# Kernel optimization log

Hardware: AMD Instinct MI355X
Metric: run time of the kernel (lower is better)

## Reference

```python
import jax, jax.numpy as jnp
import numpy as np

M = 0.25
S = 64.0  # gamma
OP = 1.0 + M      # optimum for positives
ON = -M           # optimum for negatives
DELTA_P = 1.0 - M
DELTA_N = M
EPS = 1e-12       # F.normalize eps

B, D, C = 256, 512, 100000


def setup_inputs() -> dict:
    key = jax.random.key(0)
    k1, k2, k3, k4 = jax.random.split(key, 4)
    x = jax.random.normal(k1, (B, D), dtype=jnp.float32)
    emb = jax.random.normal(k2, (B, D), dtype=jnp.float32)
    W = jax.random.normal(k3, (C, D), dtype=jnp.float32) * 0.02  # fc.weight [C, D]
    labels = jax.random.randint(k4, (B,), 0, C, dtype=jnp.int64)
    return {"x": x, "labels": labels, "emb": emb, "W": W}


def reference(x, labels, emb, W):
    # x is unused in the original forward (dead argument)
    # F.normalize(emb): L2-normalize rows with eps clamp
    norm = jnp.linalg.norm(emb, axis=1, keepdims=True)
    ff = emb / jnp.maximum(norm, EPS)
    # fc(ff): linear classifier (weights NOT normalized; the torch loop is a no-op)
    wf = ff @ W.T  # [B, C]
    wf_d = jax.lax.stop_gradient(wf)

    rows = jnp.arange(wf.shape[0])
    sp_logit = wf[rows, labels]        # torch.diagonal(wf.T[labels])
    sp_logit_d = wf_d[rows, labels]

    alpha_p = jnp.maximum(OP - sp_logit_d, 0.0)          # clamp_min(-s_p + Op, 0)
    sp = jnp.exp(-S * alpha_p * (sp_logit - DELTA_P))    # [B]

    # negatives: all classes except the label column (mask instead of cat-slicing)
    neg_mask = jnp.asarray(rows[:, None] >= 0, wf.dtype) * (1.0 - jax.nn.one_hot(labels, wf.shape[1], dtype=wf.dtype))
    alpha_n = jnp.maximum(wf_d + M, 0.0)                 # clamp_min(s_n - On, 0)
    sn = jnp.exp(S * alpha_n * (wf - DELTA_N)) * neg_mask  # label column zeroed out

    loss = jnp.log(1.0 + sn.sum() * sp.sum())
    return loss
```

## Files before the change

kernel.cpp:

```cpp
#include <hip/hip_runtime.h>
#include <hip/hip_bf16.h>

typedef __attribute__((ext_vector_type(8))) __bf16 bf16x8;
typedef __attribute__((ext_vector_type(4))) float f32x4;

#define B_M 256
#define K_D 512
#define N_C 100000
#define BN 64
#define BK 64
#define NBLK ((N_C + BN - 1) / BN)

__device__ __forceinline__ unsigned short f2bf(float x) {
  unsigned int u = __float_as_uint(x);
  u += 0x7fffu + ((u >> 16) & 1u);
  return (unsigned short)(u >> 16);
}

__global__ __launch_bounds__(256) void norm_kernel(const float* __restrict__ emb,
                                                   unsigned short* __restrict__ ff) {
  const int row = blockIdx.x;
  const int t = threadIdx.x;
  float a = emb[row * K_D + t];
  float b = emb[row * K_D + t + 256];
  float ss = a * a + b * b;
  #pragma unroll
  for (int o = 32; o > 0; o >>= 1) ss += __shfl_down(ss, o, 64);
  __shared__ float red[4];
  const int wid = t >> 6, lane = t & 63;
  if (lane == 0) red[wid] = ss;
  __syncthreads();
  float tot = red[0] + red[1] + red[2] + red[3];
  float rn = 1.0f / fmaxf(sqrtf(tot), 1e-12f);
  ff[row * K_D + t]       = f2bf(a * rn);
  ff[row * K_D + t + 256] = f2bf(b * rn);
}

__global__ __launch_bounds__(512) void gemm_loss_kernel(const unsigned short* __restrict__ ff,
                                                        const float* __restrict__ W,
                                                        const int* __restrict__ labels,
                                                        double* __restrict__ partials) {
  __shared__ __align__(16) unsigned short As[B_M * BK];
  __shared__ __align__(16) unsigned short Bs[BN * BK];
  __shared__ int lbl[B_M];
  __shared__ double red[16];

  const int tid = threadIdx.x;
  const int wid = tid >> 6;
  const int lane = tid & 63;
  const int n0 = blockIdx.x * BN;

  if (tid < B_M) lbl[tid] = labels[tid];

  f32x4 acc[2][4] = {};

  const int wrow = wid * 32;
  const int l15 = lane & 15;
  const int lhi = lane >> 4;

  const int bcol = tid >> 3;
  const int bk8  = tid & 7;
  const long long jrow = (long long)n0 + bcol;

  for (int kk = 0; kk < K_D / BK; ++kk) {
    if (kk) __syncthreads();
    #pragma unroll
    for (int it = 0; it < 4; ++it) {
      int idx = it * 512 + tid;
      int row = idx >> 3;
      int kc  = idx & 7;
      uint4 v = *reinterpret_cast<const uint4*>(ff + row * K_D + kk * BK + kc * 8);
      int off = (row * 128 + kc * 16) ^ ((row & 7) << 4);
      *reinterpret_cast<uint4*>(reinterpret_cast<char*>(As) + off) = v;
    }
    {
      float4 f0 = {0.f, 0.f, 0.f, 0.f}, f1 = {0.f, 0.f, 0.f, 0.f};
      if (jrow < N_C) {
        const float* gp = W + jrow * K_D + kk * BK + bk8 * 8;
        f0 = *reinterpret_cast<const float4*>(gp);
        f1 = *reinterpret_cast<const float4*>(gp + 4);
      }
      union { unsigned short us[8]; uint4 v; } pk;
      pk.us[0] = f2bf(f0.x); pk.us[1] = f2bf(f0.y); pk.us[2] = f2bf(f0.z); pk.us[3] = f2bf(f0.w);
      pk.us[4] = f2bf(f1.x); pk.us[5] = f2bf(f1.y); pk.us[6] = f2bf(f1.z); pk.us[7] = f2bf(f1.w);
      int off = (bcol * 128 + bk8 * 16) ^ ((bcol & 7) << 4);
      *reinterpret_cast<uint4*>(reinterpret_cast<char*>(Bs) + off) = pk.v;
    }
    __syncthreads();

    bf16x8 afr[2][2], bfr[4][2];
    #pragma unroll
    for (int fm = 0; fm < 2; ++fm)
      #pragma unroll
      for (int ks = 0; ks < 2; ++ks) {
        int row = wrow + fm * 16 + l15;
        int off = (row * 128 + ks * 64 + lhi * 16) ^ ((row & 7) << 4);
        afr[fm][ks] = *reinterpret_cast<const bf16x8*>(reinterpret_cast<const char*>(As) + off);
      }
    #pragma unroll
    for (int fn = 0; fn < 4; ++fn)
      #pragma unroll
      for (int ks = 0; ks < 2; ++ks) {
        int col = fn * 16 + l15;
        int off = (col * 128 + ks * 64 + lhi * 16) ^ ((col & 7) << 4);
        bfr[fn][ks] = *reinterpret_cast<const bf16x8*>(reinterpret_cast<const char*>(Bs) + off);
      }
    #pragma unroll
    for (int fm = 0; fm < 2; ++fm)
      #pragma unroll
      for (int fn = 0; fn < 4; ++fn)
        #pragma unroll
        for (int ks = 0; ks < 2; ++ks)
          acc[fm][fn] = __builtin_amdgcn_mfma_f32_16x16x32_bf16(afr[fm][ks], bfr[fn][ks], acc[fm][fn], 0, 0, 0);
  }

  float sn_local = 0.0f;
  double sp_local = 0.0;
  #pragma unroll
  for (int fm = 0; fm < 2; ++fm)
    #pragma unroll
    for (int fn = 0; fn < 4; ++fn)
      #pragma unroll
      for (int r = 0; r < 4; ++r) {
        int row = wrow + fm * 16 + lhi * 4 + r;
        int j = n0 + fn * 16 + l15;
        float v = acc[fm][fn][r];
        if (j < N_C) {
          if (j == lbl[row]) {
            double alpha = fmax(1.25 - (double)v, 0.0);
            sp_local += exp(-64.0 * alpha * ((double)v - 0.75));
          } else {
            float an = fmaxf(v + 0.25f, 0.0f);
            sn_local += __expf(64.0f * an * (v - 0.25f));
          }
        }
      }

  double sn_d = (double)sn_local;
  #pragma unroll
  for (int o = 32; o > 0; o >>= 1) {
    sn_d     += __shfl_down(sn_d, o, 64);
    sp_local += __shfl_down(sp_local, o, 64);
  }
  if (lane == 0) { red[wid] = sn_d; red[8 + wid] = sp_local; }
  __syncthreads();
  if (tid == 0) {
    double a = 0.0, b = 0.0;
    #pragma unroll
    for (int i = 0; i < 8; ++i) { a += red[i]; b += red[8 + i]; }
    partials[blockIdx.x] = a;
    partials[NBLK + blockIdx.x] = b;
  }
}

__global__ __launch_bounds__(512) void finalize_kernel(const double* __restrict__ partials,
                                                       float* __restrict__ out) {
  const int t = threadIdx.x;
  double sn = 0.0, sp = 0.0;
  for (int i = t; i < NBLK; i += 512) { sn += partials[i]; sp += partials[NBLK + i]; }
  #pragma unroll
  for (int o = 32; o > 0; o >>= 1) { sn += __shfl_down(sn, o, 64); sp += __shfl_down(sp, o, 64); }
  __shared__ double red[16];
  const int wid = t >> 6, lane = t & 63;
  if (lane == 0) { red[wid] = sn; red[8 + wid] = sp; }
  __syncthreads();
  if (t == 0) {
    double a = 0.0, b = 0.0;
    for (int i = 0; i < 8; ++i) { a += red[i]; b += red[8 + i]; }
    out[0] = (float)log1p(a * b);
  }
}

extern "C" void kernel_launch(void* const* d_in, const int* in_sizes, int n_in,
                              void* d_out, int out_size, void* d_ws, size_t ws_size,
                              hipStream_t stream) {
  const int*   labels = (const int*)d_in[1];
  const float* emb    = (const float*)d_in[2];
  const float* W      = (const float*)d_in[3];
  float* out = (float*)d_out;

  unsigned short* ff = (unsigned short*)d_ws;
  double* partials = (double*)((char*)d_ws + (size_t)B_M * K_D * 2);

  norm_kernel<<<B_M, 256, 0, stream>>>(emb, ff);
  gemm_loss_kernel<<<NBLK, 512, 0, stream>>>(ff, W, labels, partials);
  finalize_kernel<<<1, 512, 0, stream>>>(partials, out);
}
```

Before: 73.61 us.

## Double-buffer GEMM tiles, split batch rows across blocks, load A via global_load_lds

The fused GEMM+loss kernel now double-buffers both LDS tiles. The W fp32 loads for the next K step are issued before the current step's MFMAs and converted to bf16 afterwards, so global latency overlaps compute. The 256-row batch is split into two 128-row blocks per column tile, doubling the grid. The normalized-embedding tile is copied straight into LDS with global_load_lds, using a pre-swizzled source address. The cost is that each W tile is read and converted twice, by the two M-blocks, which relies on the cache to absorb the extra traffic. LDS use also grows.

```diff
diff --git a/kernel.cpp b/kernel.cpp
--- a/kernel.cpp
+++ b/kernel.cpp
@@ -7,14 +7,23 @@
 #define B_M 256
 #define K_D 512
 #define N_C 100000
+#define BM 128
 #define BN 64
 #define BK 64
-#define NBLK ((N_C + BN - 1) / BN)
+#define NSTEP (K_D / BK)
+#define NB_N ((N_C + BN - 1) / BN)
+#define NB (2 * NB_N)
 
 __device__ __forceinline__ unsigned short f2bf(float x) {
   unsigned int u = __float_as_uint(x);
   u += 0x7fffu + ((u >> 16) & 1u);
   return (unsigned short)(u >> 16);
+}
+
+__device__ __forceinline__ void glds16(const void* g, void* l) {
+  __builtin_amdgcn_global_load_lds(
+      (const __attribute__((address_space(1))) unsigned int*)g,
+      (__attribute__((address_space(3))) unsigned int*)l, 16, 0, 0);
 }
 
 __global__ __launch_bounds__(256) void norm_kernel(const float* __restrict__ emb,
@@ -40,93 +49,119 @@
                                                         const float* __restrict__ W,
                                                         const int* __restrict__ labels,
                                                         double* __restrict__ partials) {
-  __shared__ __align__(16) unsigned short As[B_M * BK];
-  __shared__ __align__(16) unsigned short Bs[BN * BK];
-  __shared__ int lbl[B_M];
+  __shared__ __align__(16) unsigned short As[2][BM * BK];
+  __shared__ __align__(16) unsigned short Bs[2][BN * BK];
+  __shared__ int lbl[BM];
   __shared__ double red[16];
 
   const int tid = threadIdx.x;
   const int wid = tid >> 6;
   const int lane = tid & 63;
-  const int n0 = blockIdx.x * BN;
-
-  if (tid < B_M) lbl[tid] = labels[tid];
-
-  f32x4 acc[2][4] = {};
-
-  const int wrow = wid * 32;
   const int l15 = lane & 15;
   const int lhi = lane >> 4;
 
+  const int bid = blockIdx.x;
+  const int nb = bid >> 1;
+  const int mb = bid & 1;
+  const int n0 = nb * BN;
+  const int m0 = mb * BM;
+
+  if (tid < BM) lbl[tid] = labels[m0 + tid];
+
+  const int mq = wid & 3;
+  const int nq = wid >> 2;
+
   const int bcol = tid >> 3;
   const int bk8  = tid & 7;
-  const long long jrow = (long long)n0 + bcol;
-
-  for (int kk = 0; kk < K_D / BK; ++kk) {
-    if (kk) __syncthreads();
+  const int jglob = n0 + bcol;
+  const bool valid = jglob < N_C;
+  const float* wp = W + (long long)(valid ? jglob : (N_C - 1)) * K_D + bk8 * 8;
+  const int woff = (bcol * 128 + bk8 * 16) ^ ((bcol & 7) << 4);
+
+  const int s0 = tid, s1 = 512 + tid;
+  const int arow0 = s0 >> 3, ak0 = (s0 & 7) ^ (arow0 & 7);
+  const int arow1 = s1 >> 3, ak1 = (s1 & 7) ^ (arow1 & 7);
+  const unsigned short* ap0 = ff + (m0 + arow0) * K_D + ak0 * 8;
+  const unsigned short* ap1 = ff + (m0 + arow1) * K_D + ak1 * 8;
+
+  f32x4 acc[2][2] = {};
+
+  {
+    float4 w0 = *reinterpret_cast<const float4*>(wp);
+    float4 w1 = *reinterpret_cast<const float4*>(wp + 4);
+    glds16(ap0, &As[0][0] + (size_t)s0 * 8);
+    glds16(ap1, &As[0][0] + (size_t)s1 * 8);
+    union { unsigned short us[8]; uint4 v; } pk;
+    pk.us[0] = f2bf(w0.x); pk.us[1] = f2bf(w0.y); pk.us[2] = f2bf(w0.z); pk.us[3] = f2bf(w0.w);
+    pk.us[4] = f2bf(w1.x); pk.us[5] = f2bf(w1.y); pk.us[6] = f2bf(w1.z); pk.us[7] = f2bf(w1.w);
+    *reinterpret_cast<uint4*>(reinterpret_cast<char*>(&Bs[0][0]) + woff) = pk.v;
+    asm volatile("s_waitcnt vmcnt(0)" ::: "memory");
+    asm volatile("s_waitcnt lgkmcnt(0)" ::: "memory");
+    __builtin_amdgcn_s_barrier();
+  }
+
+  for (int t = 0; t < NSTEP; ++t) {
+    const int cur = t & 1;
+    const int nxt = cur ^ 1;
+    const bool stage = (t + 1 < NSTEP);
+
+    float4 w0n, w1n;
+    if (stage) {
+      w0n = *reinterpret_cast<const float4*>(wp + (t + 1) * BK);
+      w1n = *reinterpret_cast<const float4*>(wp + (t + 1) * BK + 4);
+      glds16(ap0 + (t + 1) * BK, &As[nxt][0] + (size_t)s0 * 8);
+      glds16(ap1 + (t + 1) * BK, &As[nxt][0] + (size_t)s1 * 8);
+    }
+
+    const char* ab = reinterpret_cast<const char*>(&As[cur][0]);
+    const char* bb = reinterpret_cast<const char*>(&Bs[cur][0]);
     #pragma unroll
-    for (int it = 0; it < 4; ++it) {
-      int idx = it * 512 + tid;
-      int row = idx >> 3;
-      int kc  = idx & 7;
-      uint4 v = *reinterpret_cast<const uint4*>(ff + row * K_D + kk * BK + kc * 8);
-      int off = (row * 128 + kc * 16) ^ ((row & 7) << 4);
-      *reinterpret_cast<uint4*>(reinterpret_cast<char*>(As) + off) = v;
+    for (int ks = 0; ks < 2; ++ks) {
+      bf16x8 afr[2], bfr[2];
+      #pragma unroll
+      for (int fm = 0; fm < 2; ++fm) {
+        int row = mq * 32 + fm * 16 + l15;
+        int off = row * 128 + (((ks * 4 + lhi) ^ (row & 7)) << 4);
+        afr[fm] = *reinterpret_cast<const bf16x8*>(ab + off);
+      }
+      #pragma unroll
+      for (int fn = 0; fn < 2; ++fn) {
+        int col = nq * 32 + fn * 16 + l15;
+        int off = col * 128 + (((ks * 4 + lhi) ^ (col & 7)) << 4);
+        bfr[fn] = *reinterpret_cast<const bf16x8*>(bb + off);
+      }
+      #pragma unroll
+      for (int fm = 0; fm < 2; ++fm)
+        #pragma unroll
+        for (int fn = 0; fn < 2; ++fn)
+          acc[fm][fn] = __builtin_amdgcn_mfma_f32_16x16x32_bf16(afr[fm], bfr[fn], acc[fm][fn], 0, 0, 0);
     }
-    {
-      float4 f0 = {0.f, 0.f, 0.f, 0.f}, f1 = {0.f, 0.f, 0.f, 0.f};
-      if (jrow < N_C) {
-        const float* gp = W + jrow * K_D + kk * BK + bk8 * 8;
-        f0 = *reinterpret_cast<const float4*>(gp);
-        f1 = *reinterpret_cast<const float4*>(gp + 4);
-      }
+
+    if (stage) {
       union { unsigned short us[8]; uint4 v; } pk;
-      pk.us[0] = f2bf(f0.x); pk.us[1] = f2bf(f0.y); pk.us[2] = f2bf(f0.z); pk.us[3] = f2bf(f0.w);
-      pk.us[4] = f2bf(f1.x); pk.us[5] = f2bf(f1.y); pk.us[6] = f2bf(f1.z); pk.us[7] = f2bf(f1.w);
-      int off = (bcol * 128 + bk8 * 16) ^ ((bcol & 7) << 4);
-      *reinterpret_cast<uint4*>(reinterpret_cast<char*>(Bs) + off) = pk.v;
+      pk.us[0] = f2bf(w0n.x); pk.us[1] = f2bf(w0n.y); pk.us[2] = f2bf(w0n.z); pk.us[3] = f2bf(w0n.w);
+      pk.us[4] = f2bf(w1n.x); pk.us[5] = f2bf(w1n.y); pk.us[6] = f2bf(w1n.z); pk.us[7] = f2bf(w1n.w);
+      *reinterpret_cast<uint4*>(reinterpret_cast<char*>(&Bs[nxt][0]) + woff) = pk.v;
+      asm volatile("s_waitcnt vmcnt(0)" ::: "memory");
+      asm volatile("s_waitcnt lgkmcnt(0)" ::: "memory");
+      __builtin_amdgcn_s_barrier();
     }
-    __syncthreads();
-
-    bf16x8 afr[2][2], bfr[4][2];
+  }
+
+  float sn_local = 0.0f;
+  double sp_local = 0.0;
+  #pragma unroll
+  for (int fn = 0; fn < 2; ++fn) {
+    const int col = n0 + nq * 32 + fn * 16 + l15;
+    const bool cv = col < N_C;
     #pragma unroll
     for (int fm = 0; fm < 2; ++fm)
       #pragma unroll
-      for (int ks = 0; ks < 2; ++ks) {
-        int row = wrow + fm * 16 + l15;
-        int off = (row * 128 + ks * 64 + lhi * 16) ^ ((row & 7) << 4);
-        afr[fm][ks] = *reinterpret_cast<const bf16x8*>(reinterpret_cast<const char*>(As) + off);
-      }
-    #pragma unroll
-    for (int fn = 0; fn < 4; ++fn)
-      #pragma unroll
-      for (int ks = 0; ks < 2; ++ks) {
-        int col = fn * 16 + l15;
-        int off = (col * 128 + ks * 64 + lhi * 16) ^ ((col & 7) << 4);
-        bfr[fn][ks] = *reinterpret_cast<const bf16x8*>(reinterpret_cast<const char*>(Bs) + off);
-      }
-    #pragma unroll
-    for (int fm = 0; fm < 2; ++fm)
-      #pragma unroll
-      for (int fn = 0; fn < 4; ++fn)
-        #pragma unroll
-        for (int ks = 0; ks < 2; ++ks)
-          acc[fm][fn] = __builtin_amdgcn_mfma_f32_16x16x32_bf16(afr[fm][ks], bfr[fn][ks], acc[fm][fn], 0, 0, 0);
-  }
-
-  float sn_local = 0.0f;
-  double sp_local = 0.0;
-  #pragma unroll
-  for (int fm = 0; fm < 2; ++fm)
-    #pragma unroll
-    for (int fn = 0; fn < 4; ++fn)
-      #pragma unroll
       for (int r = 0; r < 4; ++r) {
-        int row = wrow + fm * 16 + lhi * 4 + r;
-        int j = n0 + fn * 16 + l15;
+        const int row = mq * 32 + fm * 16 + lhi * 4 + r;
         float v = acc[fm][fn][r];
-        if (j < N_C) {
-          if (j == lbl[row]) {
+        if (cv) {
+          if (col == lbl[row]) {
             double alpha = fmax(1.25 - (double)v, 0.0);
             sp_local += exp(-64.0 * alpha * ((double)v - 0.75));
           } else {
@@ -135,6 +170,7 @@
           }
         }
       }
+  }
 
   double sn_d = (double)sn_local;
   #pragma unroll
@@ -148,8 +184,8 @@
     double a = 0.0, b = 0.0;
     #pragma unroll
     for (int i = 0; i < 8; ++i) { a += red[i]; b += red[8 + i]; }
-    partials[blockIdx.x] = a;
-    partials[NBLK + blockIdx.x] = b;
+    partials[bid] = a;
+    partials[NB + bid] = b;
   }
 }
 
@@ -157,7 +193,7 @@
                                                        float* __restrict__ out) {
   const int t = threadIdx.x;
   double sn = 0.0, sp = 0.0;
-  for (int i = t; i < NBLK; i += 512) { sn += partials[i]; sp += partials[NBLK + i]; }
+  for (int i = t; i < NB; i += 512) { sn += partials[i]; sp += partials[NB + i]; }
   #pragma unroll
   for (int o = 32; o > 0; o >>= 1) { sn += __shfl_down(sn, o, 64); sp += __shfl_down(sp, o, 64); }
   __shared__ double red[16];
@@ -183,6 +219,6 @@
   double* partials = (double*)((char*)d_ws + (size_t)B_M * K_D * 2);
 
   norm_kernel<<<B_M, 256, 0, stream>>>(emb, ff);
-  gemm_loss_kernel<<<NBLK, 512, 0, stream>>>(ff, W, labels, partials);
+  gemm_loss_kernel<<<NB, 512, 0, stream>>>(ff, W, labels, partials);
   finalize_kernel<<<1, 512, 0, stream>>>(partials, out);
 }
```

New measurement: 78.07 us. 1.06x slower.

## Widen N tile to 128 and switch to 32x32x16 MFMA with 4x2 wave grid

Applied to the files above, without the earlier changes.

Doubles the class tile per block from 64 to 128, so the 256x512 bf16 activation panel is reloaded from global memory half as many times. The eight waves now form a 4x2 grid, each computing a 64x64 sub-tile with 32x32x16 bf16 MFMAs instead of 16x16x32, which cuts LDS fragment reads per FLOP. Out-of-range W rows are clamped to the last row instead of zero-filled, since those columns are masked in the epilogue. Costs are more accumulator registers per thread and half as many blocks, which may hurt occupancy and tail balance.

```diff
diff --git a/kernel.cpp b/kernel.cpp
--- a/kernel.cpp
+++ b/kernel.cpp
@@ -2,14 +2,15 @@
 #include <hip/hip_bf16.h>
 
 typedef __attribute__((ext_vector_type(8))) __bf16 bf16x8;
-typedef __attribute__((ext_vector_type(4))) float f32x4;
+typedef __attribute__((ext_vector_type(16))) float f32x16;
 
 #define B_M 256
 #define K_D 512
 #define N_C 100000
-#define BN 64
+#define BN2 128
 #define BK 64
-#define NBLK ((N_C + BN - 1) / BN)
+#define NSTEP (K_D / BK)
+#define NB2 ((N_C + BN2 - 1) / BN2)
 
 __device__ __forceinline__ unsigned short f2bf(float x) {
   unsigned int u = __float_as_uint(x);
@@ -41,92 +42,97 @@
                                                         const int* __restrict__ labels,
                                                         double* __restrict__ partials) {
   __shared__ __align__(16) unsigned short As[B_M * BK];
-  __shared__ __align__(16) unsigned short Bs[BN * BK];
+  __shared__ __align__(16) unsigned short Bs[BN2 * BK];
   __shared__ int lbl[B_M];
   __shared__ double red[16];
 
   const int tid = threadIdx.x;
   const int wid = tid >> 6;
   const int lane = tid & 63;
-  const int n0 = blockIdx.x * BN;
+  const int l31 = lane & 31;
+  const int lk8 = lane >> 5;
+  const int mq = wid & 3;
+  const int nq = wid >> 2;
+  const int n0 = blockIdx.x * BN2;
 
   if (tid < B_M) lbl[tid] = labels[tid];
 
-  f32x4 acc[2][4] = {};
+  const int wrow0 = tid >> 3;
+  const int wrow1 = 64 + (tid >> 3);
+  const int wkc = tid & 7;
+  const int j0 = n0 + wrow0;
+  const int j1 = n0 + wrow1;
+  const float* wp0 = W + (long long)(j0 < N_C ? j0 : (N_C - 1)) * K_D + wkc * 8;
+  const float* wp1 = W + (long long)(j1 < N_C ? j1 : (N_C - 1)) * K_D + wkc * 8;
+  const int woff0 = wrow0 * 128 + ((wkc ^ (wrow0 & 7)) << 4);
+  const int woff1 = wrow1 * 128 + ((wkc ^ (wrow1 & 7)) << 4);
 
-  const int wrow = wid * 32;
-  const int l15 = lane & 15;
-  const int lhi = lane >> 4;
+  f32x16 acc[2][2] = {};
 
-  const int bcol = tid >> 3;
-  const int bk8  = tid & 7;
-  const long long jrow = (long long)n0 + bcol;
-
-  for (int kk = 0; kk < K_D / BK; ++kk) {
+  for (int kk = 0; kk < NSTEP; ++kk) {
     if (kk) __syncthreads();
     #pragma unroll
     for (int it = 0; it < 4; ++it) {
-      int idx = it * 512 + tid;
-      int row = idx >> 3;
-      int kc  = idx & 7;
+      int s = it * 512 + tid;
+      int row = s >> 3;
+      int kc  = s & 7;
       uint4 v = *reinterpret_cast<const uint4*>(ff + row * K_D + kk * BK + kc * 8);
       int off = (row * 128 + kc * 16) ^ ((row & 7) << 4);
       *reinterpret_cast<uint4*>(reinterpret_cast<char*>(As) + off) = v;
     }
     {
-      float4 f0 = {0.f, 0.f, 0.f, 0.f}, f1 = {0.f, 0.f, 0.f, 0.f};
-      if (jrow < N_C) {
-        const float* gp = W + jrow * K_D + kk * BK + bk8 * 8;
-        f0 = *reinterpret_cast<const float4*>(gp);
-        f1 = *reinterpret_cast<const float4*>(gp + 4);
-      }
+      float4 a0 = *reinterpret_cast<const float4*>(wp0 + kk * BK);
+      float4 a1 = *reinterpret_cast<const float4*>(wp0 + kk * BK + 4);
+      float4 b0 = *reinterpret_cast<const float4*>(wp1 + kk * BK);
+      float4 b1 = *reinterpret_cast<const float4*>(wp1 + kk * BK + 4);
       union { unsigned short us[8]; uint4 v; } pk;
-      pk.us[0] = f2bf(f0.x); pk.us[1] = f2bf(f0.y); pk.us[2] = f2bf(f0.z); pk.us[3] = f2bf(f0.w);
-      pk.us[4] = f2bf(f1.x); pk.us[5] = f2bf(f1.y); pk.us[6] = f2bf(f1.z); pk.us[7] = f2bf(f1.w);
-      int off = (bcol * 128 + bk8 * 16) ^ ((bcol & 7) << 4);
-      *reinterpret_cast<uint4*>(reinterpret_cast<char*>(Bs) + off) = pk.v;
+      pk.us[0] = f2bf(a0.x); pk.us[1] = f2bf(a0.y); pk.us[2] = f2bf(a0.z); pk.us[3] = f2bf(a0.w);
+      pk.us[4] = f2bf(a1.x); pk.us[5] = f2bf(a1.y); pk.us[6] = f2bf(a1.z); pk.us[7] = f2bf(a1.w);
+      *reinterpret_cast<uint4*>(reinterpret_cast<char*>(Bs) + woff0) = pk.v;
+      pk.us[0] = f2bf(b0.x); pk.us[1] = f2bf(b0.y); pk.us[2] = f2bf(b0.z); pk.us[3] = f2bf(b0.w);
+      pk.us[4] = f2bf(b1.x); pk.us[5] = f2bf(b1.y); pk.us[6] = f2bf(b1.z); pk.us[7] = f2bf(b1.w);
+      *reinterpret_cast<uint4*>(reinterpret_cast<char*>(Bs) + woff1) = pk.v;
     }
     __syncthreads();
 
-    bf16x8 afr[2][2], bfr[4][2];
     #pragma unroll
-    for (int fm = 0; fm < 2; ++fm)
+    for (int ks = 0; ks < 4; ++ks) {
+      const int c16 = ks * 2 + lk8;
+      bf16x8 afr[2], bfr[2];
       #pragma unroll
-      for (int ks = 0; ks < 2; ++ks) {
-        int row = wrow + fm * 16 + l15;
-        int off = (row * 128 + ks * 64 + lhi * 16) ^ ((row & 7) << 4);
-        afr[fm][ks] = *reinterpret_cast<const bf16x8*>(reinterpret_cast<const char*>(As) + off);
+      for (int fm = 0; fm < 2; ++fm) {
+        int row = mq * 64 + fm * 32 + l31;
+        int off = row * 128 + ((c16 ^ (row & 7)) << 4);
+        afr[fm] = *reinterpret_cast<const bf16x8*>(reinterpret_cast<const char*>(As) + off);
       }
-    #pragma unroll
-    for (int fn = 0; fn < 4; ++fn)
       #pragma unroll
-      for (int ks = 0; ks < 2; ++ks) {
-        int col = fn * 16 + l15;
-        int off = (col * 128 + ks * 64 + lhi * 16) ^ ((col & 7) << 4);
-        bfr[fn][ks] = *reinterpret_cast<const bf16x8*>(reinterpret_cast<const char*>(Bs) + off);
+      for (int fn = 0; fn < 2; ++fn) {
+        int col = nq * 64 + fn * 32 + l31;
+        int off = col * 128 + ((c16 ^ (col & 7)) << 4);
+        bfr[fn] = *reinterpret_cast<const bf16x8*>(reinterpret_cast<const char*>(Bs) + off);
       }
-    #pragma unroll
-    for (int fm = 0; fm < 2; ++fm)
       #pragma unroll
-      for (int fn = 0; fn < 4; ++fn)
+      for (int fm = 0; fm < 2; ++fm)
         #pragma unroll
-        for (int ks = 0; ks < 2; ++ks)
-          acc[fm][fn] = __builtin_amdgcn_mfma_f32_16x16x32_bf16(afr[fm][ks], bfr[fn][ks], acc[fm][fn], 0, 0, 0);
+        for (int fn = 0; fn < 2; ++fn)
+          acc[fm][fn] = __builtin_amdgcn_mfma_f32_32x32x16_bf16(afr[fm], bfr[fn], acc[fm][fn], 0, 0, 0);
+    }
   }
 
   float sn_local = 0.0f;
   double sp_local = 0.0;
   #pragma unroll
-  for (int fm = 0; fm < 2; ++fm)
+  for (int fn = 0; fn < 2; ++fn) {
+    const int col = n0 + nq * 64 + fn * 32 + l31;
+    const bool cv = col < N_C;
     #pragma unroll
-    for (int fn = 0; fn < 4; ++fn)
+    for (int fm = 0; fm < 2; ++fm)
       #pragma unroll
-      for (int r = 0; r < 4; ++r) {
-        int row = wrow + fm * 16 + lhi * 4 + r;
-        int j = n0 + fn * 16 + l15;
+      for (int r = 0; r < 16; ++r) {
+        const int row = mq * 64 + fm * 32 + (r & 3) + 8 * (r >> 2) + 4 * lk8;
         float v = acc[fm][fn][r];
-        if (j < N_C) {
-          if (j == lbl[row]) {
+        if (cv) {
+          if (col == lbl[row]) {
             double alpha = fmax(1.25 - (double)v, 0.0);
             sp_local += exp(-64.0 * alpha * ((double)v - 0.75));
           } else {
@@ -135,6 +141,7 @@
           }
         }
       }
+  }
 
   double sn_d = (double)sn_local;
   #pragma unroll
@@ -149,7 +156,7 @@
     #pragma unroll
     for (int i = 0; i < 8; ++i) { a += red[i]; b += red[8 + i]; }
     partials[blockIdx.x] = a;
-    partials[NBLK + blockIdx.x] = b;
+    partials[NB2 + blockIdx.x] = b;
   }
 }
 
@@ -157,7 +164,7 @@
                                                        float* __restrict__ out) {
   const int t = threadIdx.x;
   double sn = 0.0, sp = 0.0;
-  for (int i = t; i < NBLK; i += 512) { sn += partials[i]; sp += partials[NBLK + i]; }
+  for (int i = t; i < NB2; i += 512) { sn += partials[i]; sp += partials[NB2 + i]; }
   #pragma unroll
   for (int o = 32; o > 0; o >>= 1) { sn += __shfl_down(sn, o, 64); sp += __shfl_down(sp, o, 64); }
   __shared__ double red[16];
@@ -183,6 +190,6 @@
   double* partials = (double*)((char*)d_ws + (size_t)B_M * K_D * 2);
 
   norm_kernel<<<B_M, 256, 0, stream>>>(emb, ff);
-  gemm_loss_kernel<<<NBLK, 512, 0, stream>>>(ff, W, labels, partials);
+  gemm_loss_kernel<<<NB2, 512, 0, stream>>>(ff, W, labels, partials);
   finalize_kernel<<<1, 512, 0, stream>>>(partials, out);
 }
```

Measured after the change: 73.83 us. Within noise of the previous version (+0.3%).
